# Kernel optimization log

Hardware: AMD Instinct MI355X
Metric: run time of the kernel (lower is better)

## Reference

```python
import jax, jax.numpy as jnp
import numpy as np

B, C_IN, C_OUT = 16, 64, 32
V_HI, V_LO, K = 163842, 40962, 7  # ico order-7 / order-6 vertex counts, 1-ring neighborhood size


def setup_inputs() -> dict:
    key = jax.random.key(0)
    k1, k2, k3, k4, k5 = jax.random.split(key, 5)
    x = jax.random.normal(k1, (B, C_IN, V_LO), dtype=jnp.float32)
    W = jax.random.normal(k2, (C_OUT, C_IN), dtype=jnp.float32) * 0.02
    b = jnp.zeros((C_OUT,), dtype=jnp.float32)
    max_pool_indices = jax.random.randint(k3, (B, C_OUT, V_LO), 0, K, dtype=jnp.int64 if jax.config.jax_enable_x64 else jnp.int32)
    up_neigh_indices = jax.random.randint(k4, (V_HI, K), 0, V_HI, dtype=jnp.int32)
    down_indices = jax.random.randint(k5, (V_LO,), 0, V_HI, dtype=jnp.int32)
    return {"x": x, "W": W, "b": b, "max_pool_indices": max_pool_indices,
            "up_neigh_indices": up_neigh_indices, "down_indices": down_indices}


def reference(x, W, b, max_pool_indices, up_neigh_indices, down_indices):
    # neigh_indices = up_neigh_indices[down_indices]  -> (V_LO, K)
    neigh_indices = up_neigh_indices[down_indices]
    n_samples, _, n_raw = x.shape
    # fc applied per-vertex on the feature axis: (B, C_IN, V) -> (B, C_OUT, V)
    h = jnp.einsum('bcv,oc->bov', x, W) + b[None, :, None]
    n_feats = W.shape[0]
    n_vertices = up_neigh_indices.shape[0]
    # vertices_indices[b, f, v] = neigh_indices[v, max_pool_indices[b, f, v]]
    vert_idx = neigh_indices[jnp.arange(n_raw)[None, None, :], max_pool_indices]  # (B, C_OUT, V_LO)
    # feats_indices exactly as original: floor(linspace(0, n_feats, n_raw*n_feats)), last -= 1
    feats_idx = np.floor(np.linspace(0.0, float(n_feats), num=n_raw * n_feats))
    feats_idx[-1] -= 1
    feats_idx = jnp.asarray(feats_idx.astype(np.int32))  # (C_OUT*V_LO,)
    h_flat = h.reshape(n_samples, -1)            # (B, C_OUT*V_LO), layout (feat, vertex)
    vert_flat = vert_idx.reshape(n_samples, -1)  # (B, C_OUT*V_LO)
    y = jnp.zeros((n_samples, n_feats, n_vertices), dtype=h.dtype)
    y = y.at[jnp.arange(n_samples)[:, None], feats_idx[None, :], vert_flat].set(h_flat)
    return y
```

## Files before the change

### kernel.cpp

```cpp
#include <hip/hip_runtime.h>
#include <hip/hip_bf16.h>
#include <stdint.h>

#define B_    16
#define C_IN  64
#define C_OUT 32
#define V_HI  163842
#define V_LO  40962
#define K_    7
#define TOTAL_E (V_LO * K_)
#define NPART 641

#define S_MP_BYTES 40968
#define GATHER_LDS (S_MP_BYTES + V_LO * 2 + 4)

__global__ __launch_bounds__(256) void compute_h_k(
    const float* __restrict__ x, const float* __restrict__ W,
    const float* __restrict__ bias, __hip_bfloat16* __restrict__ h)
{
    __shared__ float sW[C_OUT * C_IN];
    __shared__ float sB[C_OUT];
    int t = threadIdx.x;
    for (int i = t; i < C_OUT * C_IN; i += 256) sW[i] = W[i];
    if (t < C_OUT) sB[t] = bias[t];
    __syncthreads();

    int b = blockIdx.y;
    int v = blockIdx.x * 256 + t;
    if (v >= V_LO) return;

    const float* xp = x + (size_t)b * C_IN * V_LO + v;
    float acc[C_OUT];
#pragma unroll
    for (int o = 0; o < C_OUT; ++o) acc[o] = 0.0f;

    for (int c = 0; c < C_IN; ++c) {
        float xv = xp[(size_t)c * V_LO];
#pragma unroll
        for (int o = 0; o < C_OUT; ++o)
            acc[o] += xv * sW[o * C_IN + c];
    }

    __hip_bfloat16* hp = h + (size_t)b * C_OUT * V_LO + v;
#pragma unroll
    for (int o = 0; o < C_OUT; ++o)
        hp[(size_t)o * V_LO] = __float2bfloat16(acc[o] + sB[o]);
}

__global__ __launch_bounds__(256) void count_k(
    const int* __restrict__ up, const int* __restrict__ down,
    unsigned* __restrict__ cnt)
{
    int v = blockIdx.x * 256 + threadIdx.x;
    if (v >= V_LO) return;
    int d = down[v];
    const int* row = up + (size_t)d * K_;
    for (int k = 0; k < K_; ++k)
        atomicAdd(&cnt[row[k]], 1u);
}

__global__ __launch_bounds__(256) void blocksum_k(
    const unsigned* __restrict__ cnt, unsigned* __restrict__ partials)
{
    __shared__ unsigned s[256];
    int i = blockIdx.x * 256 + threadIdx.x;
    unsigned v = (i < V_HI) ? cnt[i] : 0u;
    s[threadIdx.x] = v;
    __syncthreads();
    for (int off = 128; off > 0; off >>= 1) {
        if (threadIdx.x < off) s[threadIdx.x] += s[threadIdx.x + off];
        __syncthreads();
    }
    if (threadIdx.x == 0) partials[blockIdx.x] = s[0];
}

__global__ __launch_bounds__(1024) void scanpart_k(unsigned* __restrict__ partials)
{
    __shared__ unsigned s[1024];
    int t = threadIdx.x;
    unsigned v = (t < NPART) ? partials[t] : 0u;
    s[t] = v;
    __syncthreads();
    for (int off = 1; off < 1024; off <<= 1) {
        unsigned add = (t >= off) ? s[t - off] : 0u;
        __syncthreads();
        s[t] += add;
        __syncthreads();
    }
    if (t < NPART) partials[t] = s[t] - v;
}

__global__ __launch_bounds__(256) void addoff_k(
    const unsigned* __restrict__ cnt, const unsigned* __restrict__ partials,
    unsigned* __restrict__ offsets, unsigned* __restrict__ cursor)
{
    __shared__ unsigned s[256];
    int t = threadIdx.x;
    int i = blockIdx.x * 256 + t;
    unsigned c = (i < V_HI) ? cnt[i] : 0u;
    s[t] = c;
    __syncthreads();
    for (int off = 1; off < 256; off <<= 1) {
        unsigned add = (t >= off) ? s[t - off] : 0u;
        __syncthreads();
        s[t] += add;
        __syncthreads();
    }
    unsigned excl = s[t] - c + partials[blockIdx.x];
    if (i < V_HI) { offsets[i] = excl; cursor[i] = excl; }
    if (i == 0) offsets[V_HI] = (unsigned)TOTAL_E;
}

__global__ __launch_bounds__(256) void scatter_k(
    const int* __restrict__ up, const int* __restrict__ down,
    unsigned* __restrict__ cursor, unsigned* __restrict__ entries)
{
    int v = blockIdx.x * 256 + threadIdx.x;
    if (v >= V_LO) return;
    int d = down[v];
    const int* row = up + (size_t)d * K_;
    for (int k = 0; k < K_; ++k) {
        int u = row[k];
        unsigned pos = atomicAdd(&cursor[u], 1u);
        entries[pos] = ((unsigned)v << 3) | (unsigned)k;
    }
}

__global__ __launch_bounds__(1024) void gather_out_k(
    const unsigned* __restrict__ offsets, const unsigned* __restrict__ entries,
    const int* __restrict__ mp, const ushort* __restrict__ h,
    float* __restrict__ out)
{
    extern __shared__ char smem[];
    unsigned char* s_mp = (unsigned char*)smem;
    ushort*        s_h  = (ushort*)(smem + S_MP_BYTES);

    int pair = blockIdx.x;
    const int*    mpp = mp  + (size_t)pair * V_LO;
    const ushort* hp  = h   + (size_t)pair * V_LO;
    float*        op  = out + (size_t)pair * V_HI;

    for (int i = threadIdx.x; i < V_LO; i += 1024) {
        s_mp[i] = (unsigned char)mpp[i];
        s_h[i]  = hp[i];
    }
    __syncthreads();

    for (int u = threadIdx.x; u < V_HI; u += 1024) {
        unsigned s0 = offsets[u];
        unsigned s1 = offsets[u + 1];
        int best = -1;
        for (unsigned e = s0; e < s1; ++e) {
            unsigned p = entries[e];
            int v = (int)(p >> 3);
            int k = (int)(p & 7u);
            if (s_mp[v] == (unsigned char)k && v > best) best = v;
        }
        float r = 0.0f;
        if (best >= 0)
            r = __uint_as_float(((unsigned)s_h[best]) << 16);
        op[u] = r;
    }
}

extern "C" void kernel_launch(void* const* d_in, const int* in_sizes, int n_in,
                              void* d_out, int out_size, void* d_ws, size_t ws_size,
                              hipStream_t stream)
{
    const float* x    = (const float*)d_in[0];
    const float* W    = (const float*)d_in[1];
    const float* bias = (const float*)d_in[2];
    const int*   mp   = (const int*)d_in[3];
    const int*   up   = (const int*)d_in[4];
    const int*   down = (const int*)d_in[5];
    float* out = (float*)d_out;

    char* ws = (char*)d_ws;
    const size_t H_BYTES   = (size_t)B_ * C_OUT * V_LO * sizeof(__hip_bfloat16);
    const size_t CNT_OFF   = H_BYTES;
    const size_t OFF_OFF   = CNT_OFF + (size_t)V_HI * 4;
    const size_t CUR_OFF   = OFF_OFF + (size_t)(V_HI + 1) * 4;
    const size_t ENT_OFF   = CUR_OFF + (size_t)V_HI * 4;
    const size_t PART_OFF  = ENT_OFF + (size_t)TOTAL_E * 4;

    __hip_bfloat16* h = (__hip_bfloat16*)ws;
    unsigned* cnt     = (unsigned*)(ws + CNT_OFF);
    unsigned* offsets = (unsigned*)(ws + OFF_OFF);
    unsigned* cursor  = (unsigned*)(ws + CUR_OFF);
    unsigned* entries = (unsigned*)(ws + ENT_OFF);
    unsigned* partials= (unsigned*)(ws + PART_OFF);

    (void)hipFuncSetAttribute((const void*)gather_out_k,
                              hipFuncAttributeMaxDynamicSharedMemorySize,
                              GATHER_LDS);

    hipMemsetAsync(cnt, 0, (size_t)V_HI * 4, stream);

    {
        dim3 grid((V_LO + 255) / 256, B_);
        compute_h_k<<<grid, 256, 0, stream>>>(x, W, bias, h);
    }

    {
        int vblk = (V_LO + 255) / 256;
        count_k<<<vblk, 256, 0, stream>>>(up, down, cnt);
        blocksum_k<<<NPART, 256, 0, stream>>>(cnt, partials);
        scanpart_k<<<1, 1024, 0, stream>>>(partials);
        addoff_k<<<NPART, 256, 0, stream>>>(cnt, partials, offsets, cursor);
        scatter_k<<<vblk, 256, 0, stream>>>(up, down, cursor, entries);
    }

    gather_out_k<<<B_ * C_OUT, 1024, GATHER_LDS, stream>>>(offsets, entries, mp, (const ushort*)h, out);
}
```

Measured before the change: 1.030 ms.

## Sort gather threads by in-degree per tile, shrink LDS, vectorize fc kernel

Adds a per-tile counting sort of high-res vertices by incoming-edge count, so that threads in a wavefront walk similar-length entry lists and branch divergence in the gather loop drops. The gather kernel no longer stages h in LDS and reads it straight from global memory, which cuts LDS use to about 41KB and may allow higher occupancy. The fc kernel now computes 4 vertices per thread with vectorized loads to get more reuse of the weights. The trade-offs are scattered output writes through the permutation, an extra kernel launch, and uncached global reads of h.

```diff
diff --git a/kernel.cpp b/kernel.cpp
--- a/kernel.cpp
+++ b/kernel.cpp
@@ -10,13 +10,14 @@
 #define K_    7
 #define TOTAL_E (V_LO * K_)
 #define NPART 641
-
-#define S_MP_BYTES 40968
-#define GATHER_LDS (S_MP_BYTES + V_LO * 2 + 4)
+#define NTILE 161
+
+typedef float f4 __attribute__((ext_vector_type(4)));
+typedef float f2 __attribute__((ext_vector_type(2)));
 
 __global__ __launch_bounds__(256) void compute_h_k(
     const float* __restrict__ x, const float* __restrict__ W,
-    const float* __restrict__ bias, __hip_bfloat16* __restrict__ h)
+    const float* __restrict__ bias, ushort* __restrict__ h)
 {
     __shared__ float sW[C_OUT * C_IN];
     __shared__ float sB[C_OUT];
@@ -25,26 +26,69 @@
     if (t < C_OUT) sB[t] = bias[t];
     __syncthreads();
 
-    int b = blockIdx.y;
-    int v = blockIdx.x * 256 + t;
-    if (v >= V_LO) return;
-
-    const float* xp = x + (size_t)b * C_IN * V_LO + v;
-    float acc[C_OUT];
-#pragma unroll
-    for (int o = 0; o < C_OUT; ++o) acc[o] = 0.0f;
-
-    for (int c = 0; c < C_IN; ++c) {
-        float xv = xp[(size_t)c * V_LO];
+    int b  = blockIdx.y;
+    int v0 = (blockIdx.x * 256 + t) * 4;
+    if (v0 >= V_LO) return;
+
+    const float* xb = x + (size_t)b * C_IN * V_LO;
+
+    float acc[C_OUT][4];
+#pragma unroll
+    for (int o = 0; o < C_OUT; ++o)
+#pragma unroll
+        for (int j = 0; j < 4; ++j) acc[o][j] = 0.0f;
+
+    if (v0 + 4 <= V_LO) {
+        for (int c0 = 0; c0 < C_IN; c0 += 4) {
+            float xv[4][4];
+#pragma unroll
+            for (int cc = 0; cc < 4; ++cc) {
+                const float* p = xb + (size_t)(c0 + cc) * V_LO + v0;
+                f2 a = *(const f2*)p;
+                f2 bq = *(const f2*)(p + 2);
+                xv[cc][0] = a[0]; xv[cc][1] = a[1];
+                xv[cc][2] = bq[0]; xv[cc][3] = bq[1];
+            }
+#pragma unroll
+            for (int o = 0; o < C_OUT; ++o) {
+                f4 w = *(const f4*)(&sW[o * C_IN + c0]);
+#pragma unroll
+                for (int j = 0; j < 4; ++j)
+                    acc[o][j] += w[0]*xv[0][j] + w[1]*xv[1][j]
+                               + w[2]*xv[2][j] + w[3]*xv[3][j];
+            }
+        }
+        ushort* hp = h + (size_t)b * C_OUT * V_LO + v0;
+#pragma unroll
+        for (int o = 0; o < C_OUT; ++o) {
+            ushort us[4];
+#pragma unroll
+            for (int j = 0; j < 4; ++j) {
+                __hip_bfloat16 bf = __float2bfloat16(acc[o][j] + sB[o]);
+                us[j] = *(ushort*)&bf;
+            }
+            ushort2 p0; p0.x = us[0]; p0.y = us[1];
+            ushort2 p1; p1.x = us[2]; p1.y = us[3];
+            *(ushort2*)(hp + (size_t)o * V_LO)     = p0;
+            *(ushort2*)(hp + (size_t)o * V_LO + 2) = p1;
+        }
+    } else {
+        int nv = V_LO - v0;
+        for (int c = 0; c < C_IN; ++c)
+            for (int j = 0; j < nv; ++j) {
+                float xs = xb[(size_t)c * V_LO + v0 + j];
+#pragma unroll
+                for (int o = 0; o < C_OUT; ++o)
+                    acc[o][j] += xs * sW[o * C_IN + c];
+            }
+        ushort* hp = h + (size_t)b * C_OUT * V_LO + v0;
 #pragma unroll
         for (int o = 0; o < C_OUT; ++o)
-            acc[o] += xv * sW[o * C_IN + c];
-    }
-
-    __hip_bfloat16* hp = h + (size_t)b * C_OUT * V_LO + v;
-#pragma unroll
-    for (int o = 0; o < C_OUT; ++o)
-        hp[(size_t)o * V_LO] = __float2bfloat16(acc[o] + sB[o]);
+            for (int j = 0; j < nv; ++j) {
+                __hip_bfloat16 bf = __float2bfloat16(acc[o][j] + sB[o]);
+                hp[(size_t)o * V_LO + j] = *(ushort*)&bf;
+            }
+    }
 }
 
 __global__ __launch_bounds__(256) void count_k(
@@ -126,40 +170,64 @@
     }
 }
 
+__global__ __launch_bounds__(1024) void permtile_k(
+    const unsigned* __restrict__ cnt, ushort* __restrict__ perm)
+{
+    __shared__ unsigned hist[16];
+    __shared__ unsigned base[16];
+    int t = threadIdx.x;
+    int u = blockIdx.x * 1024 + t;
+    if (t < 16) hist[t] = 0;
+    __syncthreads();
+    bool valid = (u < V_HI);
+    unsigned c = 0, rank = 0;
+    if (valid) {
+        c = cnt[u];
+        if (c > 15u) c = 15u;
+        rank = atomicAdd(&hist[c], 1u);
+    }
+    __syncthreads();
+    if (t == 0) {
+        unsigned r = 0;
+        for (int i = 0; i < 16; ++i) { base[i] = r; r += hist[i]; }
+    }
+    __syncthreads();
+    if (valid) perm[blockIdx.x * 1024 + base[c] + rank] = (ushort)t;
+}
+
 __global__ __launch_bounds__(1024) void gather_out_k(
     const unsigned* __restrict__ offsets, const unsigned* __restrict__ entries,
     const int* __restrict__ mp, const ushort* __restrict__ h,
-    float* __restrict__ out)
-{
-    extern __shared__ char smem[];
-    unsigned char* s_mp = (unsigned char*)smem;
-    ushort*        s_h  = (ushort*)(smem + S_MP_BYTES);
+    const ushort* __restrict__ perm, float* __restrict__ out)
+{
+    __shared__ unsigned char s_mp[V_LO + 2];
 
     int pair = blockIdx.x;
     const int*    mpp = mp  + (size_t)pair * V_LO;
     const ushort* hp  = h   + (size_t)pair * V_LO;
     float*        op  = out + (size_t)pair * V_HI;
 
-    for (int i = threadIdx.x; i < V_LO; i += 1024) {
+    for (int i = threadIdx.x; i < V_LO; i += 1024)
         s_mp[i] = (unsigned char)mpp[i];
-        s_h[i]  = hp[i];
-    }
-    __syncthreads();
-
-    for (int u = threadIdx.x; u < V_HI; u += 1024) {
-        unsigned s0 = offsets[u];
-        unsigned s1 = offsets[u + 1];
-        int best = -1;
-        for (unsigned e = s0; e < s1; ++e) {
-            unsigned p = entries[e];
-            int v = (int)(p >> 3);
-            int k = (int)(p & 7u);
-            if (s_mp[v] == (unsigned char)k && v > best) best = v;
+    __syncthreads();
+
+    for (int tb = 0; tb < V_HI; tb += 1024) {
+        int slot = tb + threadIdx.x;
+        if (slot < V_HI) {
+            int pu = tb + (int)perm[slot];
+            unsigned s0 = offsets[pu];
+            unsigned s1 = offsets[pu + 1];
+            int best = -1;
+            for (unsigned e = s0; e < s1; ++e) {
+                unsigned p = entries[e];
+                int v = (int)(p >> 3);
+                if (s_mp[v] == (p & 7u) && v > best) best = v;
+            }
+            float r = 0.0f;
+            if (best >= 0)
+                r = __uint_as_float(((unsigned)hp[best]) << 16);
+            op[pu] = r;
         }
-        float r = 0.0f;
-        if (best >= 0)
-            r = __uint_as_float(((unsigned)s_h[best]) << 16);
-        op[u] = r;
     }
 }
 
@@ -176,28 +244,26 @@
     float* out = (float*)d_out;
 
     char* ws = (char*)d_ws;
-    const size_t H_BYTES   = (size_t)B_ * C_OUT * V_LO * sizeof(__hip_bfloat16);
+    const size_t H_BYTES   = (size_t)B_ * C_OUT * V_LO * 2;
     const size_t CNT_OFF   = H_BYTES;
     const size_t OFF_OFF   = CNT_OFF + (size_t)V_HI * 4;
     const size_t CUR_OFF   = OFF_OFF + (size_t)(V_HI + 1) * 4;
     const size_t ENT_OFF   = CUR_OFF + (size_t)V_HI * 4;
     const size_t PART_OFF  = ENT_OFF + (size_t)TOTAL_E * 4;
-
-    __hip_bfloat16* h = (__hip_bfloat16*)ws;
+    const size_t PERM_OFF  = PART_OFF + (size_t)NPART * 4 + 64;
+
+    ushort*   h       = (ushort*)ws;
     unsigned* cnt     = (unsigned*)(ws + CNT_OFF);
     unsigned* offsets = (unsigned*)(ws + OFF_OFF);
     unsigned* cursor  = (unsigned*)(ws + CUR_OFF);
     unsigned* entries = (unsigned*)(ws + ENT_OFF);
     unsigned* partials= (unsigned*)(ws + PART_OFF);
-
-    (void)hipFuncSetAttribute((const void*)gather_out_k,
-                              hipFuncAttributeMaxDynamicSharedMemorySize,
-                              GATHER_LDS);
+    ushort*   perm    = (ushort*)(ws + PERM_OFF);
 
     hipMemsetAsync(cnt, 0, (size_t)V_HI * 4, stream);
 
     {
-        dim3 grid((V_LO + 255) / 256, B_);
+        dim3 grid((V_LO + 1023) / 1024, B_);
         compute_h_k<<<grid, 256, 0, stream>>>(x, W, bias, h);
     }
 
@@ -208,7 +274,8 @@
         scanpart_k<<<1, 1024, 0, stream>>>(partials);
         addoff_k<<<NPART, 256, 0, stream>>>(cnt, partials, offsets, cursor);
         scatter_k<<<vblk, 256, 0, stream>>>(up, down, cursor, entries);
-    }
-
-    gather_out_k<<<B_ * C_OUT, 1024, GATHER_LDS, stream>>>(offsets, entries, mp, (const ushort*)h, out);
-}
+        permtile_k<<<NTILE, 1024, 0, stream>>>(cnt, perm);
+    }
+
+    gather_out_k<<<B_ * C_OUT, 1024, 0, stream>>>(offsets, entries, mp, h, perm, out);
+}
```

Result: slower. 1.500 ms (+45.6%).
